# Kernel optimization log

Hardware: AMD Instinct MI355X
Metric: run time of the kernel (lower is better)

Reference implementation:

```python
import jax, jax.numpy as jnp
import numpy as np

B, S, HID = 2, 2048, 2048
N_HEADS, N_KV, HD = 16, 4, 128
ROPE_THETA = 10000.0


def _rope_cos_sin(seq_len, head_dim, theta):
    freqs = 1.0 / (theta ** (jnp.arange(0, head_dim, 2, dtype=jnp.float32) / head_dim))  # [hd/2]
    ang = jnp.arange(seq_len, dtype=jnp.float32)[:, None] * freqs[None, :]  # [S, hd/2]
    return jnp.cos(ang), jnp.sin(ang)


def _apply_rope(x, cos, sin):
    # x: [B, S, H, hd]; interleaved pairs rotation (llama/qwen complex form)
    xs = x.reshape(*x.shape[:-1], HD // 2, 2)
    x1, x2 = xs[..., 0], xs[..., 1]
    c = cos[None, :, None, :]
    s = sin[None, :, None, :]
    o1 = x1 * c - x2 * s
    o2 = x1 * s + x2 * c
    return jnp.stack([o1, o2], axis=-1).reshape(x.shape)


def setup_inputs() -> dict:
    key = jax.random.key(0)
    ks = jax.random.split(key, 8)
    std = 0.02
    return {
        "hidden_states": jax.random.normal(ks[0], (B, S, HID), jnp.float32),
        "q_w": jax.random.normal(ks[1], (HID, N_HEADS * HD), jnp.float32) * std,
        "q_b": jnp.zeros((N_HEADS * HD,), jnp.float32),
        "k_w": jax.random.normal(ks[2], (HID, N_KV * HD), jnp.float32) * std,
        "k_b": jnp.zeros((N_KV * HD,), jnp.float32),
        "v_w": jax.random.normal(ks[3], (HID, N_KV * HD), jnp.float32) * std,
        "v_b": jnp.zeros((N_KV * HD,), jnp.float32),
        "o_w": jax.random.normal(ks[4], (N_HEADS * HD, HID), jnp.float32) * std,
    }


def reference(hidden_states, q_w, q_b, k_w, k_b, v_w, v_b, o_w):
    b, s, _ = hidden_states.shape
    q = (hidden_states @ q_w + q_b).reshape(b, s, N_HEADS, HD)
    k = (hidden_states @ k_w + k_b).reshape(b, s, N_KV, HD)
    v = (hidden_states @ v_w + v_b).reshape(b, s, N_KV, HD)

    cos, sin = _rope_cos_sin(s, HD, ROPE_THETA)
    q = _apply_rope(q, cos, sin)
    k = _apply_rope(k, cos, sin)

    # GQA: repeat kv heads to match query heads
    rep = N_HEADS // N_KV
    k = jnp.repeat(k, rep, axis=2)  # [b, s, N_HEADS, hd]
    v = jnp.repeat(v, rep, axis=2)

    scale = 1.0 / jnp.sqrt(jnp.asarray(HD, jnp.float32))
    scores = jnp.einsum("bqhd,bkhd->bhqk", q, k) * scale  # [b, H, S, S]
    causal = jnp.tril(jnp.ones((s, s), dtype=bool))
    scores = jnp.where(causal[None, None], scores, jnp.finfo(scores.dtype).min)
    probs = jax.nn.softmax(scores, axis=-1)
    attn = jnp.einsum("bhqk,bkhd->bqhd", probs, v).reshape(b, s, N_HEADS * HD)
    return attn @ o_w
```

## Files before the change

kernel.cpp:

```cpp
#include <hip/hip_runtime.h>
#include <hip/hip_bf16.h>
#include <math.h>

#define BB 2
#define SS 2048
#define HID 2048
#define NH 16
#define NKV 4
#define HD 128

typedef __bf16 bf16_t;
typedef bf16_t bf16x8 __attribute__((ext_vector_type(8)));
typedef bf16_t bf16x4 __attribute__((ext_vector_type(4)));
typedef float f32x4 __attribute__((ext_vector_type(4)));

#define AS1 __attribute__((address_space(1)))
#define AS3 __attribute__((address_space(3)))

#define CSC 0.12746231410988061f

__device__ __forceinline__ void gload16(const bf16_t* g, bf16_t* lds) {
    __builtin_amdgcn_global_load_lds((const AS1 void*)g, (AS3 void*)lds, 16, 0, 0);
}

__global__ __launch_bounds__(256) void rope_tab_kernel(float2* __restrict__ tab)
{
    int i = blockIdx.x * 256 + threadIdx.x;
    int j = i & 63, s = i >> 6;
    float freq = expf(-(float)j * 0.14391156831212787f);
    float sn, cs;
    sincosf((float)s * freq, &sn, &cs);
    tab[i] = make_float2(cs, sn);
}

__global__ __launch_bounds__(256) void cast_hidden_kernel(
    const float* __restrict__ X, bf16_t* __restrict__ Xb)
{
    size_t i = (size_t)(blockIdx.x * 256 + threadIdx.x) * 8;
    float4 a = *reinterpret_cast<const float4*>(X + i);
    float4 b = *reinterpret_cast<const float4*>(X + i + 4);
    bf16x8 v = { (bf16_t)a.x, (bf16_t)a.y, (bf16_t)a.z, (bf16_t)a.w,
                 (bf16_t)b.x, (bf16_t)b.y, (bf16_t)b.z, (bf16_t)b.w };
    *reinterpret_cast<bf16x8*>(Xb + i) = v;
}

__global__ __launch_bounds__(256) void transpose_cast_kernel(
    const float* __restrict__ q_w, const float* __restrict__ k_w,
    const float* __restrict__ v_w, const float* __restrict__ o_w,
    bf16_t* __restrict__ Wq, bf16_t* __restrict__ Wk,
    bf16_t* __restrict__ Wv, bf16_t* __restrict__ Wo)
{
    __shared__ float tile[32][33];
    const float* W; bf16_t* Wt; int N;
    switch (blockIdx.z) {
        case 0: W = q_w; Wt = Wq; N = 2048; break;
        case 1: W = k_w; Wt = Wk; N = 512;  break;
        case 2: W = v_w; Wt = Wv; N = 512;  break;
        default: W = o_w; Wt = Wo; N = 2048; break;
    }
    int n0 = blockIdx.x * 32, k0 = blockIdx.y * 32;
    if (n0 >= N) return;
    int c = threadIdx.x & 31, r0 = threadIdx.x >> 5;
    #pragma unroll
    for (int rr = 0; rr < 32; rr += 8)
        tile[r0 + rr][c] = W[(size_t)(k0 + r0 + rr) * N + n0 + c];
    __syncthreads();
    #pragma unroll
    for (int rr = 0; rr < 32; rr += 8)
        Wt[(size_t)(n0 + r0 + rr) * HID + k0 + c] = (bf16_t)tile[c][r0 + rr];
}

__device__ __forceinline__ void gemm_core_bf16(
    const bf16_t* __restrict__ A, const bf16_t* __restrict__ Bt,
    int m0, int n0, bf16_t* As, bf16_t* Bs, f32x4 acc[4][4])
{
    const int t = threadIdx.x;
    const int w = t >> 6, lane = t & 63, lo = lane & 15, hi = lane >> 4;
    const int wr = (w >> 1) * 64, wc = (w & 1) * 64;

    for (int k0 = 0; k0 < HID; k0 += 32) {
        __syncthreads();
        #pragma unroll
        for (int i = 0; i < 2; ++i) {
            int j = t + i * 256;
            gload16(A  + (size_t)(m0 + (j >> 2)) * HID + k0 + (j & 3) * 8,
                    As + (size_t)(w * 64 + i * 256) * 8);
            gload16(Bt + (size_t)(n0 + (j >> 2)) * HID + k0 + (j & 3) * 8,
                    Bs + (size_t)(w * 64 + i * 256) * 8);
        }
        __syncthreads();
        const bf16x8* Av = reinterpret_cast<const bf16x8*>(As);
        const bf16x8* Bv = reinterpret_cast<const bf16x8*>(Bs);
        bf16x8 a[4], b[4];
        #pragma unroll
        for (int m = 0; m < 4; ++m) a[m] = Av[(wr + m * 16 + lo) * 4 + hi];
        #pragma unroll
        for (int n = 0; n < 4; ++n) b[n] = Bv[(wc + n * 16 + lo) * 4 + hi];
        #pragma unroll
        for (int m = 0; m < 4; ++m)
            #pragma unroll
            for (int n = 0; n < 4; ++n)
                acc[m][n] = __builtin_amdgcn_mfma_f32_16x16x32_bf16(
                    a[m], b[n], acc[m][n], 0, 0, 0);
    }
}

__global__ __launch_bounds__(256) void qkv_gemm_kernel(
    const bf16_t* __restrict__ X,
    const bf16_t* __restrict__ Wq, const bf16_t* __restrict__ Wk,
    const bf16_t* __restrict__ Wv,
    const float* __restrict__ qb, const float* __restrict__ kb,
    const float* __restrict__ vb,
    const float2* __restrict__ rope_tab,
    bf16_t* __restrict__ Qo, bf16_t* __restrict__ Ko, bf16_t* __restrict__ Vt)
{
    __shared__ bf16_t As[128 * 32], Bs[128 * 32];
    f32x4 acc[4][4];
    #pragma unroll
    for (int m = 0; m < 4; ++m)
        #pragma unroll
        for (int n = 0; n < 4; ++n) acc[m][n] = (f32x4){0.f, 0.f, 0.f, 0.f};

    const int bn = blockIdx.x, m0 = blockIdx.y * 128;
    const bf16_t* Bt; const float* bias; int mode, head;
    if (bn < 16)      { Bt = Wq; bias = qb; mode = 0; head = bn; }
    else if (bn < 20) { Bt = Wk; bias = kb; mode = 1; head = bn - 16; }
    else              { Bt = Wv; bias = vb; mode = 2; head = bn - 20; }

    gemm_core_bf16(X, Bt, m0, head * 128, As, Bs, acc);

    const int t = threadIdx.x, w = t >> 6, lane = t & 63;
    const int lo = lane & 15, hi = lane >> 4;
    const int wr = (w >> 1) * 64, wc = (w & 1) * 64;

    #pragma unroll
    for (int n = 0; n < 4; ++n) {
        const int d = wc + n * 16 + lo;
        const float bv = bias[head * 128 + d];
        const int jj = d >> 1;
        #pragma unroll
        for (int m = 0; m < 4; ++m) {
            #pragma unroll
            for (int r = 0; r < 4; ++r) {
                const int row = m0 + wr + m * 16 + hi * 4 + r;
                const int b = row >> 11, s = row & 2047;
                float v = acc[m][n][r] + bv;
                if (mode < 2) {
                    float2 cs = rope_tab[s * 64 + jj];
                    float p = __shfl_xor(v, 1);
                    v = (d & 1) ? (p * cs.y + v * cs.x)
                                : (v * cs.x - p * cs.y);
                    if (mode == 0)
                        Qo[((size_t)(b * NH + head) * SS + s) * HD + d] =
                            (bf16_t)(v * CSC);
                    else
                        Ko[((size_t)(b * NKV + head) * SS + s) * HD + d] = (bf16_t)v;
                } else {
                    Vt[((size_t)(b * NKV + head) * HD + d) * SS + s] = (bf16_t)v;
                }
            }
        }
    }
}

__global__ __launch_bounds__(256) void oproj_gemm_kernel(
    const bf16_t* __restrict__ Ab, const bf16_t* __restrict__ Wo,
    float* __restrict__ out)
{
    __shared__ bf16_t As[128 * 32], Bs[128 * 32];
    f32x4 acc[4][4];
    #pragma unroll
    for (int m = 0; m < 4; ++m)
        #pragma unroll
        for (int n = 0; n < 4; ++n) acc[m][n] = (f32x4){0.f, 0.f, 0.f, 0.f};

    const int m0 = blockIdx.y * 128, n0 = blockIdx.x * 128;
    gemm_core_bf16(Ab, Wo, m0, n0, As, Bs, acc);

    const int t = threadIdx.x, w = t >> 6, lane = t & 63;
    const int lo = lane & 15, hi = lane >> 4;
    const int wr = (w >> 1) * 64, wc = (w & 1) * 64;
    #pragma unroll
    for (int m = 0; m < 4; ++m)
        #pragma unroll
        for (int n = 0; n < 4; ++n)
            #pragma unroll
            for (int r = 0; r < 4; ++r) {
                int row = m0 + wr + m * 16 + hi * 4 + r;
                int col = n0 + wc + n * 16 + lo;
                out[(size_t)row * HID + col] = acc[m][n][r];
            }
}

__global__ __launch_bounds__(256, 4) void attn_kernel(
    const bf16_t* __restrict__ Q, const bf16_t* __restrict__ K,
    const bf16_t* __restrict__ Vt, bf16_t* __restrict__ O)
{
    __shared__ bf16_t Kbuf[2][4096];
    __shared__ bf16_t Vbuf[2][4096];
    __shared__ bf16_t Ps[4][512];

    const int t = threadIdx.x, w = t >> 6, lane = t & 63;
    const int lo = lane & 15, hi = lane >> 4;
    const int bid = blockIdx.x;
    const int b    = (bid >> 2) & 1, hkv = bid & 3;
    const int h    = hkv * 4 + ((bid >> 3) & 3);
    const int ss   = 31 - (bid >> 5);
    const int q0   = ss * 64 + w * 16;
    const int dX   = (q0 + 15) >> 5;
    const int nk   = 2 * ss + 2;

    const bf16_t* Qh = Q  + (size_t)(b * NH  + h)   * SS * HD;
    const bf16_t* Kh = K  + (size_t)(b * NKV + hkv) * SS * HD;
    const bf16_t* Vh = Vt + (size_t)(b * NKV + hkv) * HD * SS;

    int preK[2], preV[2];
    #pragma unroll
    for (int i = 0; i < 2; ++i) {
        const int o = t + i * 256;
        const int krow = o >> 4;
        const int kslot = (o & 15) ^ (krow & 7);
        preK[i] = krow * HD + kslot * 8;
        const int d = o >> 2;
        const int cc = (o & 3) ^ ((d ^ (d >> 2)) & 3);
        preV[i] = d * SS + cc * 8;
    }

    bf16x8 qf[4];
    #pragma unroll
    for (int c = 0; c < 4; ++c)
        qf[c] = *reinterpret_cast<const bf16x8*>(
            Qh + (size_t)(q0 + lo) * HD + c * 32 + hi * 8);

    f32x4 of[8];
    #pragma unroll
    for (int n = 0; n < 8; ++n) of[n] = (f32x4){0.f, 0.f, 0.f, 0.f};
    float m_run = -3.0e38f, l_run = 0.f;

    #pragma unroll
    for (int i = 0; i < 2; ++i) {
        gload16(Kh + preK[i], &Kbuf[0][(w * 64 + i * 256) * 8]);
        gload16(Vh + preV[i], &Vbuf[0][(w * 64 + i * 256) * 8]);
    }

    for (int kt = 0; kt < nk; ++kt) {
        const int cur = kt & 1;
        __syncthreads();
        if (kt + 1 < nk) {
            const int kOff = (kt + 1) * 32 * HD;
            const int vOff = (kt + 1) * 32;
            #pragma unroll
            for (int i = 0; i < 2; ++i) {
                gload16(Kh + kOff + preK[i], &Kbuf[cur ^ 1][(w * 64 + i * 256) * 8]);
                gload16(Vh + vOff + preV[i], &Vbuf[cur ^ 1][(w * 64 + i * 256) * 8]);
            }
        }
        if (kt > dX) continue;

        const bf16_t* Kb = Kbuf[cur];
        f32x4 sfr[2];
        sfr[0] = (f32x4){0.f, 0.f, 0.f, 0.f};
        sfr[1] = (f32x4){0.f, 0.f, 0.f, 0.f};
        #pragma unroll
        for (int kg = 0; kg < 2; ++kg) {
            const int krow = kg * 16 + lo;
            #pragma unroll
            for (int c = 0; c < 4; ++c) {
                const int slot = (c * 4 + hi) ^ (krow & 7);
                bf16x8 kf = *reinterpret_cast<const bf16x8*>(
                    Kb + krow * 128 + slot * 8);
                sfr[kg] = __builtin_amdgcn_mfma_f32_16x16x32_bf16(
                    kf, qf[c], sfr[kg], 0, 0, 0);
            }
        }

        float s[8];
        #pragma unroll
        for (int kg = 0; kg < 2; ++kg)
            #pragma unroll
            for (int r = 0; r < 4; ++r) s[kg * 4 + r] = sfr[kg][r];
        if (kt == dX) {
            const int qrow = q0 + lo;
            #pragma unroll
            for (int kg = 0; kg < 2; ++kg)
                #pragma unroll
                for (int r = 0; r < 4; ++r)
                    if (kt * 32 + kg * 16 + hi * 4 + r > qrow)
                        s[kg * 4 + r] = -3.0e38f;
        }
        float pmax = fmaxf(fmaxf(fmaxf(s[0], s[1]), fmaxf(s[2], s[3])),
                           fmaxf(fmaxf(s[4], s[5]), fmaxf(s[6], s[7])));
        pmax = fmaxf(pmax, __shfl_xor(pmax, 16));
        pmax = fmaxf(pmax, __shfl_xor(pmax, 32));
        if (!__all(pmax - m_run <= 11.5f)) {
            float mnew = fmaxf(m_run, pmax);
            float corr = exp2f(m_run - mnew);
            m_run = mnew;
            l_run *= corr;
            #pragma unroll
            for (int r = 0; r < 4; ++r) {
                float cr = __shfl(corr, hi * 4 + r);
                #pragma unroll
                for (int n = 0; n < 8; ++n) of[n][r] *= cr;
            }
        }
        float e[8], psl = 0.f;
        #pragma unroll
        for (int i = 0; i < 8; ++i) {
            e[i] = exp2f(s[i] - m_run);
            psl += e[i];
        }
        l_run += psl;

        bf16_t* ps = Ps[w];
        #pragma unroll
        for (int kg = 0; kg < 2; ++kg) {
            bf16x4 pk;
            #pragma unroll
            for (int r = 0; r < 4; ++r) pk[r] = (bf16_t)e[kg * 4 + r];
            const int oct = kg * 2 + (hi >> 1);
            *reinterpret_cast<bf16x4*>(ps + (oct * 16 + lo) * 8 + (hi & 1) * 4) = pk;
        }
        bf16x8 pf = *reinterpret_cast<const bf16x8*>(ps + lane * 8);

        const bf16_t* Vb = Vbuf[cur];
        #pragma unroll
        for (int n = 0; n < 8; ++n) {
            const int d = n * 16 + lo;
            const int cc = hi ^ ((d ^ (d >> 2)) & 3);
            bf16x8 vf = *reinterpret_cast<const bf16x8*>(Vb + d * 32 + cc * 8);
            of[n] = __builtin_amdgcn_mfma_f32_16x16x32_bf16(
                pf, vf, of[n], 0, 0, 0);
        }
    }

    float lr = l_run + __shfl_xor(l_run, 16);
    lr += __shfl_xor(lr, 32);
    #pragma unroll
    for (int r = 0; r < 4; ++r) {
        float inv = 1.0f / __shfl(lr, hi * 4 + r);
        bf16_t* dst = O + ((size_t)(b * SS + q0 + hi * 4 + r)) * HID + h * HD;
        #pragma unroll
        for (int n = 0; n < 8; ++n)
            dst[n * 16 + lo] = (bf16_t)(of[n][r] * inv);
    }
}

extern "C" void kernel_launch(void* const* d_in, const int* in_sizes, int n_in,
                              void* d_out, int out_size, void* d_ws, size_t ws_size,
                              hipStream_t stream)
{
    const float* hidden = (const float*)d_in[0];
    const float* q_w    = (const float*)d_in[1];
    const float* q_b    = (const float*)d_in[2];
    const float* k_w    = (const float*)d_in[3];
    const float* k_b    = (const float*)d_in[4];
    const float* v_w    = (const float*)d_in[5];
    const float* v_b    = (const float*)d_in[6];
    const float* o_w    = (const float*)d_in[7];
    float* out = (float*)d_out;

    bf16_t* p  = (bf16_t*)d_ws;
    bf16_t* Xb = p; p += (size_t)4096 * 2048;
    bf16_t* Wq = p; p += (size_t)2048 * 2048;
    bf16_t* Wk = p; p += (size_t)512  * 2048;
    bf16_t* Wv = p; p += (size_t)512  * 2048;
    bf16_t* Wo = p; p += (size_t)2048 * 2048;
    bf16_t* Qb = p; p += (size_t)BB * NH  * SS * HD;
    bf16_t* Kb = p; p += (size_t)BB * NKV * SS * HD;
    bf16_t* Vt = p; p += (size_t)BB * NKV * HD * SS;
    bf16_t* Ab = p; p += (size_t)4096 * 2048;
    float2* rope_tab = (float2*)p;

    rope_tab_kernel<<<512, 256, 0, stream>>>(rope_tab);
    cast_hidden_kernel<<<4096, 256, 0, stream>>>(hidden, Xb);
    transpose_cast_kernel<<<dim3(64, 64, 4), 256, 0, stream>>>(
        q_w, k_w, v_w, o_w, Wq, Wk, Wv, Wo);
    qkv_gemm_kernel<<<dim3(24, 32), 256, 0, stream>>>(
        Xb, Wq, Wk, Wv, q_b, k_b, v_b, rope_tab, Qb, Kb, Vt);
    attn_kernel<<<1024, 256, 0, stream>>>(Qb, Kb, Vt, Ab);
    oproj_gemm_kernel<<<dim3(16, 32), 256, 0, stream>>>(Ab, Wo, out);
}
```

Baseline: 337.9 us.

## Replace GEMM core with 256x256 eight-wave pipelined tile and swizzled LDS

```diff
diff --git a/kernel.cpp b/kernel.cpp
--- a/kernel.cpp
+++ b/kernel.cpp
@@ -8,6 +8,7 @@
 #define NH 16
 #define NKV 4
 #define HD 128
+#define NT 32
 
 typedef __bf16 bf16_t;
 typedef bf16_t bf16x8 __attribute__((ext_vector_type(8)));
@@ -47,16 +48,15 @@
 __global__ __launch_bounds__(256) void transpose_cast_kernel(
     const float* __restrict__ q_w, const float* __restrict__ k_w,
     const float* __restrict__ v_w, const float* __restrict__ o_w,
-    bf16_t* __restrict__ Wq, bf16_t* __restrict__ Wk,
-    bf16_t* __restrict__ Wv, bf16_t* __restrict__ Wo)
+    bf16_t* __restrict__ Wqkv, bf16_t* __restrict__ Wo)
 {
     __shared__ float tile[32][33];
     const float* W; bf16_t* Wt; int N;
     switch (blockIdx.z) {
-        case 0: W = q_w; Wt = Wq; N = 2048; break;
-        case 1: W = k_w; Wt = Wk; N = 512;  break;
-        case 2: W = v_w; Wt = Wv; N = 512;  break;
-        default: W = o_w; Wt = Wo; N = 2048; break;
+        case 0: W = q_w; Wt = Wqkv;                       N = 2048; break;
+        case 1: W = k_w; Wt = Wqkv + (size_t)2048 * HID;  N = 512;  break;
+        case 2: W = v_w; Wt = Wqkv + (size_t)2560 * HID;  N = 512;  break;
+        default: W = o_w; Wt = Wo;                        N = 2048; break;
     }
     int n0 = blockIdx.x * 32, k0 = blockIdx.y * 32;
     if (n0 >= N) return;
@@ -70,126 +70,218 @@
         Wt[(size_t)(n0 + r0 + rr) * HID + k0 + c] = (bf16_t)tile[c][r0 + rr];
 }
 
-__device__ __forceinline__ void gemm_core_bf16(
+__device__ __forceinline__ void stage_half(
+    const bf16_t* __restrict__ g, bf16_t* lds, int w, int l)
+{
+    #pragma unroll
+    for (int i = 0; i < 2; ++i) {
+        const int c = w * 64 + l + i * 512;
+        const int r = c >> 3;
+        const int s = (c & 7) ^ (r & 7);
+        gload16(g + (size_t)r * HID + s * 8, lds + (w * 64 + i * 512) * 8);
+    }
+}
+
+__device__ __forceinline__ bf16x8 ldsfrag(const bf16_t* reg, int row, int kh, int hi)
+{
+    const int slot = (kh * 4 + hi) ^ (row & 7);
+    return *reinterpret_cast<const bf16x8*>(reg + row * 64 + slot * 8);
+}
+
+#define SBAR()   __builtin_amdgcn_s_barrier()
+#define SCHED0() __builtin_amdgcn_sched_barrier(0)
+#define WAITV4() asm volatile("s_waitcnt vmcnt(4)" ::: "memory")
+
+__device__ __forceinline__ void gemm8_core(
     const bf16_t* __restrict__ A, const bf16_t* __restrict__ Bt,
-    int m0, int n0, bf16_t* As, bf16_t* Bs, f32x4 acc[4][4])
-{
-    const int t = threadIdx.x;
-    const int w = t >> 6, lane = t & 63, lo = lane & 15, hi = lane >> 4;
-    const int wr = (w >> 1) * 64, wc = (w & 1) * 64;
-
-    for (int k0 = 0; k0 < HID; k0 += 32) {
-        __syncthreads();
-        #pragma unroll
-        for (int i = 0; i < 2; ++i) {
-            int j = t + i * 256;
-            gload16(A  + (size_t)(m0 + (j >> 2)) * HID + k0 + (j & 3) * 8,
-                    As + (size_t)(w * 64 + i * 256) * 8);
-            gload16(Bt + (size_t)(n0 + (j >> 2)) * HID + k0 + (j & 3) * 8,
-                    Bs + (size_t)(w * 64 + i * 256) * 8);
-        }
-        __syncthreads();
-        const bf16x8* Av = reinterpret_cast<const bf16x8*>(As);
-        const bf16x8* Bv = reinterpret_cast<const bf16x8*>(Bs);
-        bf16x8 a[4], b[4];
-        #pragma unroll
-        for (int m = 0; m < 4; ++m) a[m] = Av[(wr + m * 16 + lo) * 4 + hi];
-        #pragma unroll
-        for (int n = 0; n < 4; ++n) b[n] = Bv[(wc + n * 16 + lo) * 4 + hi];
-        #pragma unroll
-        for (int m = 0; m < 4; ++m)
-            #pragma unroll
-            for (int n = 0; n < 4; ++n)
-                acc[m][n] = __builtin_amdgcn_mfma_f32_16x16x32_bf16(
-                    a[m], b[n], acc[m][n], 0, 0, 0);
-    }
-}
-
-__global__ __launch_bounds__(256) void qkv_gemm_kernel(
-    const bf16_t* __restrict__ X,
-    const bf16_t* __restrict__ Wq, const bf16_t* __restrict__ Wk,
-    const bf16_t* __restrict__ Wv,
+    int m0, int n0, bf16_t* Abuf, bf16_t* Bbuf, f32x4 (&acc)[8][4])
+{
+    const int t0 = threadIdx.x;
+    const int w = t0 >> 6, lane = t0 & 63, lo = lane & 15, hi = lane >> 4;
+    const int wm = w >> 2, wn = w & 3;
+    const int brow0 = (wn & 1) * 64;
+
+    const bf16_t* Ag[2] = { A  + (size_t)m0 * HID, A  + (size_t)(m0 + 128) * HID };
+    const bf16_t* Bg[2] = { Bt + (size_t)n0 * HID, Bt + (size_t)(n0 + 128) * HID };
+
+    stage_half(Ag[0],      Abuf + 0 * 8192, w, lane);
+    stage_half(Ag[1],      Abuf + 1 * 8192, w, lane);
+    stage_half(Bg[0],      Bbuf + 0 * 8192, w, lane);
+    stage_half(Bg[1],      Bbuf + 1 * 8192, w, lane);
+    stage_half(Bg[0] + 64, Bbuf + 2 * 8192, w, lane);
+    stage_half(Bg[1] + 64, Bbuf + 3 * 8192, w, lane);
+    WAITV4();
+    SBAR();
+    SCHED0();
+
+    for (int t = 0; t < NT; ++t) {
+        const int pt = t & 1, pn = pt ^ 1;
+        const int tA = (t + 1 < NT) ? t + 1 : NT - 1;
+        const int tB = (t + 2 < NT) ? t + 2 : NT - 1;
+        const bf16_t* ARg = Abuf + (pt * 2 + wm) * 8192;
+        const bf16_t* BRg = Bbuf + (pt * 2 + (wn >> 1)) * 8192;
+        bf16x8 a[4], b0[4], b1[4];
+
+        #pragma unroll
+        for (int i = 0; i < 4; ++i) a[i] = ldsfrag(ARg, i * 16 + lo, 0, hi);
+        #pragma unroll
+        for (int j = 0; j < 4; ++j) b0[j] = ldsfrag(BRg, brow0 + j * 16 + lo, 0, hi);
+        stage_half(Ag[0] + tA * 64, Abuf + (pn * 2 + 0) * 8192, w, lane);
+        SBAR();
+        __builtin_amdgcn_s_setprio(1);
+        #pragma unroll
+        for (int i = 0; i < 4; ++i)
+            #pragma unroll
+            for (int j = 0; j < 4; ++j)
+                acc[i][j] = __builtin_amdgcn_mfma_f32_16x16x32_bf16(
+                    a[i], b0[j], acc[i][j], 0, 0, 0);
+        __builtin_amdgcn_s_setprio(0);
+        SBAR();
+        SCHED0();
+
+        #pragma unroll
+        for (int i = 0; i < 4; ++i) a[i] = ldsfrag(ARg, i * 16 + lo, 1, hi);
+        #pragma unroll
+        for (int j = 0; j < 4; ++j) b1[j] = ldsfrag(BRg, brow0 + j * 16 + lo, 1, hi);
+        stage_half(Ag[1] + tA * 64, Abuf + (pn * 2 + 1) * 8192, w, lane);
+        SBAR();
+        __builtin_amdgcn_s_setprio(1);
+        #pragma unroll
+        for (int i = 0; i < 4; ++i)
+            #pragma unroll
+            for (int j = 0; j < 4; ++j)
+                acc[i][j] = __builtin_amdgcn_mfma_f32_16x16x32_bf16(
+                    a[i], b1[j], acc[i][j], 0, 0, 0);
+        __builtin_amdgcn_s_setprio(0);
+        SBAR();
+        SCHED0();
+
+        #pragma unroll
+        for (int i = 0; i < 4; ++i) a[i] = ldsfrag(ARg, 64 + i * 16 + lo, 0, hi);
+        stage_half(Bg[0] + tB * 64, Bbuf + (pt * 2 + 0) * 8192, w, lane);
+        SBAR();
+        __builtin_amdgcn_s_setprio(1);
+        #pragma unroll
+        for (int i = 0; i < 4; ++i)
+            #pragma unroll
+            for (int j = 0; j < 4; ++j)
+                acc[4 + i][j] = __builtin_amdgcn_mfma_f32_16x16x32_bf16(
+                    a[i], b0[j], acc[4 + i][j], 0, 0, 0);
+        __builtin_amdgcn_s_setprio(0);
+        SBAR();
+        SCHED0();
+
+        #pragma unroll
+        for (int i = 0; i < 4; ++i) a[i] = ldsfrag(ARg, 64 + i * 16 + lo, 1, hi);
+        stage_half(Bg[1] + tB * 64, Bbuf + (pt * 2 + 1) * 8192, w, lane);
+        SBAR();
+        __builtin_amdgcn_s_setprio(1);
+        #pragma unroll
+        for (int i = 0; i < 4; ++i)
+            #pragma unroll
+            for (int j = 0; j < 4; ++j)
+                acc[4 + i][j] = __builtin_amdgcn_mfma_f32_16x16x32_bf16(
+                    a[i], b1[j], acc[4 + i][j], 0, 0, 0);
+        __builtin_amdgcn_s_setprio(0);
+        WAITV4();
+        SBAR();
+        SCHED0();
+    }
+}
+
+__global__ __launch_bounds__(512, 2) void qkv_gemm8_kernel(
+    const bf16_t* __restrict__ X, const bf16_t* __restrict__ Wqkv,
     const float* __restrict__ qb, const float* __restrict__ kb,
-    const float* __restrict__ vb,
-    const float2* __restrict__ rope_tab,
+    const float* __restrict__ vb, const float2* __restrict__ rope_tab,
     bf16_t* __restrict__ Qo, bf16_t* __restrict__ Ko, bf16_t* __restrict__ Vt)
 {
-    __shared__ bf16_t As[128 * 32], Bs[128 * 32];
-    f32x4 acc[4][4];
-    #pragma unroll
-    for (int m = 0; m < 4; ++m)
+    __shared__ bf16_t Abuf[4 * 8192];
+    __shared__ bf16_t Bbuf[4 * 8192];
+
+    const int bid = blockIdx.x;
+    const int wg = (bid & 7) * 24 + (bid >> 3);
+    const int m0 = (wg / 12) * 256, n0 = (wg % 12) * 256;
+
+    f32x4 acc[8][4];
+    #pragma unroll
+    for (int m = 0; m < 8; ++m)
         #pragma unroll
         for (int n = 0; n < 4; ++n) acc[m][n] = (f32x4){0.f, 0.f, 0.f, 0.f};
 
-    const int bn = blockIdx.x, m0 = blockIdx.y * 128;
-    const bf16_t* Bt; const float* bias; int mode, head;
-    if (bn < 16)      { Bt = Wq; bias = qb; mode = 0; head = bn; }
-    else if (bn < 20) { Bt = Wk; bias = kb; mode = 1; head = bn - 16; }
-    else              { Bt = Wv; bias = vb; mode = 2; head = bn - 20; }
-
-    gemm_core_bf16(X, Bt, m0, head * 128, As, Bs, acc);
-
-    const int t = threadIdx.x, w = t >> 6, lane = t & 63;
+    gemm8_core(X, Wqkv, m0, n0, Abuf, Bbuf, acc);
+
+    const int t0 = threadIdx.x, w = t0 >> 6, lane = t0 & 63;
     const int lo = lane & 15, hi = lane >> 4;
-    const int wr = (w >> 1) * 64, wc = (w & 1) * 64;
-
-    #pragma unroll
-    for (int n = 0; n < 4; ++n) {
-        const int d = wc + n * 16 + lo;
-        const float bv = bias[head * 128 + d];
+    const int wm = w >> 2, wn = w & 3;
+    const int gc0 = n0 + wn * 64;
+    const int mode = (gc0 < 2048) ? 0 : (gc0 < 2560 ? 1 : 2);
+
+    #pragma unroll
+    for (int j = 0; j < 4; ++j) {
+        const int col = gc0 + j * 16 + lo;
+        float bv; int hh, d;
+        if (mode == 0)      { bv = qb[col];        hh = col >> 7;          d = col & 127; }
+        else if (mode == 1) { bv = kb[col - 2048]; hh = (col - 2048) >> 7; d = (col - 2048) & 127; }
+        else                { bv = vb[col - 2560]; hh = (col - 2560) >> 7; d = (col - 2560) & 127; }
         const int jj = d >> 1;
         #pragma unroll
-        for (int m = 0; m < 4; ++m) {
+        for (int mi = 0; mi < 8; ++mi) {
+            const int rowb = m0 + wm * 128 + (mi >> 2) * 64 + (mi & 3) * 16 + hi * 4;
             #pragma unroll
             for (int r = 0; r < 4; ++r) {
-                const int row = m0 + wr + m * 16 + hi * 4 + r;
-                const int b = row >> 11, s = row & 2047;
-                float v = acc[m][n][r] + bv;
+                const int rw = rowb + r, b = rw >> 11, s = rw & 2047;
+                float v = acc[mi][j][r] + bv;
                 if (mode < 2) {
                     float2 cs = rope_tab[s * 64 + jj];
-                    float p = __shfl_xor(v, 1);
-                    v = (d & 1) ? (p * cs.y + v * cs.x)
-                                : (v * cs.x - p * cs.y);
+                    float pp = __shfl_xor(v, 1);
+                    v = (d & 1) ? (pp * cs.y + v * cs.x)
+                                : (v * cs.x - pp * cs.y);
                     if (mode == 0)
-                        Qo[((size_t)(b * NH + head) * SS + s) * HD + d] =
+                        Qo[((size_t)(b * NH + hh) * SS + s) * HD + d] =
                             (bf16_t)(v * CSC);
                     else
-                        Ko[((size_t)(b * NKV + head) * SS + s) * HD + d] = (bf16_t)v;
+                        Ko[((size_t)(b * NKV + hh) * SS + s) * HD + d] = (bf16_t)v;
                 } else {
-                    Vt[((size_t)(b * NKV + head) * HD + d) * SS + s] = (bf16_t)v;
+                    Vt[((size_t)(b * NKV + hh) * HD + d) * SS + s] = (bf16_t)v;
                 }
             }
         }
     }
 }
 
-__global__ __launch_bounds__(256) void oproj_gemm_kernel(
+__global__ __launch_bounds__(512, 2) void oproj_gemm8_kernel(
     const bf16_t* __restrict__ Ab, const bf16_t* __restrict__ Wo,
     float* __restrict__ out)
 {
-    __shared__ bf16_t As[128 * 32], Bs[128 * 32];
-    f32x4 acc[4][4];
-    #pragma unroll
-    for (int m = 0; m < 4; ++m)
+    __shared__ bf16_t Abuf[4 * 8192];
+    __shared__ bf16_t Bbuf[4 * 8192];
+
+    const int bid = blockIdx.x;
+    const int wg = (bid & 7) * 16 + (bid >> 3);
+    const int m0 = (wg / 8) * 256, n0 = (wg % 8) * 256;
+
+    f32x4 acc[8][4];
+    #pragma unroll
+    for (int m = 0; m < 8; ++m)
         #pragma unroll
         for (int n = 0; n < 4; ++n) acc[m][n] = (f32x4){0.f, 0.f, 0.f, 0.f};
 
-    const int m0 = blockIdx.y * 128, n0 = blockIdx.x * 128;
-    gemm_core_bf16(Ab, Wo, m0, n0, As, Bs, acc);
-
-    const int t = threadIdx.x, w = t >> 6, lane = t & 63;
+    gemm8_core(Ab, Wo, m0, n0, Abuf, Bbuf, acc);
+
+    const int t0 = threadIdx.x, w = t0 >> 6, lane = t0 & 63;
     const int lo = lane & 15, hi = lane >> 4;
-    const int wr = (w >> 1) * 64, wc = (w & 1) * 64;
-    #pragma unroll
-    for (int m = 0; m < 4; ++m)
-        #pragma unroll
-        for (int n = 0; n < 4; ++n)
-            #pragma unroll
-            for (int r = 0; r < 4; ++r) {
-                int row = m0 + wr + m * 16 + hi * 4 + r;
-                int col = n0 + wc + n * 16 + lo;
-                out[(size_t)row * HID + col] = acc[m][n][r];
-            }
+    const int wm = w >> 2, wn = w & 3;
+    #pragma unroll
+    for (int mi = 0; mi < 8; ++mi) {
+        const int rowb = m0 + wm * 128 + (mi >> 2) * 64 + (mi & 3) * 16 + hi * 4;
+        #pragma unroll
+        for (int j = 0; j < 4; ++j) {
+            const int col = n0 + wn * 64 + j * 16 + lo;
+            #pragma unroll
+            for (int r = 0; r < 4; ++r)
+                out[(size_t)(rowb + r) * HID + col] = acc[mi][j][r];
+        }
+    }
 }
 
 __global__ __launch_bounds__(256, 4) void attn_kernel(
@@ -360,24 +452,22 @@
     const float* o_w    = (const float*)d_in[7];
     float* out = (float*)d_out;
 
-    bf16_t* p  = (bf16_t*)d_ws;
-    bf16_t* Xb = p; p += (size_t)4096 * 2048;
-    bf16_t* Wq = p; p += (size_t)2048 * 2048;
-    bf16_t* Wk = p; p += (size_t)512  * 2048;
-    bf16_t* Wv = p; p += (size_t)512  * 2048;
-    bf16_t* Wo = p; p += (size_t)2048 * 2048;
-    bf16_t* Qb = p; p += (size_t)BB * NH  * SS * HD;
-    bf16_t* Kb = p; p += (size_t)BB * NKV * SS * HD;
-    bf16_t* Vt = p; p += (size_t)BB * NKV * HD * SS;
-    bf16_t* Ab = p; p += (size_t)4096 * 2048;
+    bf16_t* p    = (bf16_t*)d_ws;
+    bf16_t* Xb   = p; p += (size_t)4096 * 2048;
+    bf16_t* Wqkv = p; p += (size_t)3072 * 2048;
+    bf16_t* Wo   = p; p += (size_t)2048 * 2048;
+    bf16_t* Qb   = p; p += (size_t)BB * NH  * SS * HD;
+    bf16_t* Kb   = p; p += (size_t)BB * NKV * SS * HD;
+    bf16_t* Vt   = p; p += (size_t)BB * NKV * HD * SS;
+    bf16_t* Ab   = p; p += (size_t)4096 * 2048;
     float2* rope_tab = (float2*)p;
 
     rope_tab_kernel<<<512, 256, 0, stream>>>(rope_tab);
     cast_hidden_kernel<<<4096, 256, 0, stream>>>(hidden, Xb);
     transpose_cast_kernel<<<dim3(64, 64, 4), 256, 0, stream>>>(
-        q_w, k_w, v_w, o_w, Wq, Wk, Wv, Wo);
-    qkv_gemm_kernel<<<dim3(24, 32), 256, 0, stream>>>(
-        Xb, Wq, Wk, Wv, q_b, k_b, v_b, rope_tab, Qb, Kb, Vt);
+        q_w, k_w, v_w, o_w, Wqkv, Wo);
+    qkv_gemm8_kernel<<<192, 512, 0, stream>>>(
+        Xb, Wqkv, q_b, k_b, v_b, rope_tab, Qb, Kb, Vt);
     attn_kernel<<<1024, 256, 0, stream>>>(Qb, Kb, Vt, Ab);
-    oproj_gemm_kernel<<<dim3(16, 32), 256, 0, stream>>>(Ab, Wo, out);
-}
+    oproj_gemm8_kernel<<<128, 512, 0, stream>>>(Ab, Wo, out);
+}
```

Result: slower. 366.2 us (+8.4%).
